# Kernel tuning notes

Hardware: AMD Instinct MI355X
Metric: run time of the kernel (lower is better)

The kernel has to match this reference:

```python
import jax, jax.numpy as jnp
import numpy as np

B, T, NM = 128, 2048, 8  # batch, nSteps, nMaxwell


def setup_inputs() -> dict:
    key = jax.random.key(0)
    k1, k2, k3 = jax.random.split(key, 3)
    S_e = jax.random.normal(k1, (B, T, 3, 3), dtype=jnp.float32)
    # strictly increasing times per batch element
    dt = jax.random.uniform(k2, (B, T), minval=0.01, maxval=0.1, dtype=jnp.float32)
    t = jnp.cumsum(dt, axis=1)
    # [tau_1..tau_nM, g_infy, g_1..g_nM] -> last dim 2*NM + 1
    PronyParams = jax.random.uniform(k3, (B, T, 2 * NM + 1), minval=0.1, maxval=1.0, dtype=jnp.float32)
    return {"S_e": S_e, "t": t, "PronyParams": PronyParams}


def reference(S_e, t, PronyParams):
    """Viscoelastic 2nd Piola-Kirchhoff stress via recursive Prony update.

    S_e:         [B, T, 3, 3] instantaneous elastic stress
    t:           [B, T] time
    PronyParams: [B, T, 2*nM+1] (relaxation times tau then coefficients g)
    Returns (S, S_infy, Q_sum), each [B, T, 3, 3].
    """
    nM = PronyParams.shape[-1] // 2
    tau = PronyParams[..., :nM]                      # [B,T,nM]
    g = PronyParams[..., nM:]                        # [B,T,nM+1]
    g = g / jnp.sum(g, axis=-1, keepdims=True)
    g_infy = g[..., 0:1]                             # [B,T,1]
    g_i = g[..., 1:]                                 # [B,T,nM]

    Bsz = S_e.shape[0]
    # time-major scan inputs
    xs = (
        jnp.swapaxes(t, 0, 1),      # [T,B]
        jnp.swapaxes(S_e, 0, 1),    # [T,B,3,3]
        jnp.swapaxes(tau, 0, 1),    # [T,B,nM]
        jnp.swapaxes(g_i, 0, 1),    # [T,B,nM]
    )
    init = (
        jnp.zeros((Bsz, nM, 3, 3), S_e.dtype),  # Q_0
        -t[:, 1],                                # t_prev (as in original initializer)
        jnp.zeros((Bsz, 3, 3), S_e.dtype),       # S_prev
        tau[:, 0],
        g_i[:, 0],
    )

    def step(carry, x):
        Q_p, t_p, S_p, tau_p, g_p = carry
        t_c, S_c, tau_c, g_c = x
        g_bar = 0.5 * (g_c + g_p)                 # [B,nM]
        tau_bar = 0.5 * (tau_c + tau_p)           # [B,nM]
        dt = (t_c - t_p)[:, None]                 # [B,1]
        e = jnp.exp(-0.5 * dt / tau_bar)          # exp(-dt/(2 tau_bar))
        term1 = (e * e)[..., None, None]          # exp(-dt/tau_bar), [B,nM,1,1]
        term2 = (e * g_bar)[..., None, None]      # [B,nM,1,1]
        dS = (S_c - S_p)[:, None]                 # [B,1,3,3]
        Q = term1 * Q_p + term2 * dS              # [B,nM,3,3]
        return (Q, t_c, S_c, tau_c, g_c), Q

    _, Qs = jax.lax.scan(step, init, xs)          # [T,B,nM,3,3]
    Q_sum = jnp.swapaxes(jnp.sum(Qs, axis=2), 0, 1)  # [B,T,3,3]
    S_infy = g_infy[..., None] * S_e              # [B,T,1,1] * [B,T,3,3]
    S = S_infy + Q_sum
    return (S, S_infy, Q_sum)
```

## Files before the change

### kernel.cpp

```cpp
#include <hip/hip_runtime.h>

#define T_LEN 2048
#define NMODE 8
#define NPP   17

template <int L, int G>
__global__ __launch_bounds__(256)
void phaseA(const float* __restrict__ Se,
            const float* __restrict__ tt,
            const float* __restrict__ pp,
            float* __restrict__ out,
            float* __restrict__ partR,
            float* __restrict__ partP,
            float* __restrict__ caA,
            int B) {
    constexpr int NC    = T_LEN / L;
    constexpr int NSTEP = G * L;
    constexpr int RW    = NSTEP + 1;
    constexpr int NT    = 256;
    constexpr int RAW_SZ = RW * NPP;
    constexpr int QT_SZ  = 9 * (NSTEP + 4);
    constexpr int CA_K   = L * 8 + 4;
    constexpr int UNION_SZ = (RAW_SZ > QT_SZ + G * CA_K) ? RAW_SZ
                                                         : (QT_SZ + G * CA_K);
    constexpr int AC_K  = L * 16 + 4;
    constexpr int O_AC  = UNION_SZ;
    constexpr int SROW  = NSTEP + 4;
    constexpr int O_ST  = O_AC + G * AC_K;
    constexpr int O_T   = O_ST + 9 * SROW;
    constexpr int O_INV = O_T + RW;
    constexpr int O_GI  = O_INV + RW;
    constexpr int TOTAL = O_GI + RW;

    __shared__ __align__(16) float sm[TOTAL];
    float* s_raw = sm;
    float* s_qT  = sm;
    float* s_ca  = sm + QT_SZ;
    float* s_AC  = sm + O_AC;
    float* s_ST  = sm + O_ST;
    float* s_t   = sm + O_T;
    float* s_inv = sm + O_INV;
    float* s_gi  = sm + O_GI;

    const int tid  = threadIdx.x;
    const int ngrp = NC / G;
    const int b    = blockIdx.x / ngrp;
    const int grp  = blockIdx.x % ngrp;
    const int c0   = grp * G;
    const int base = c0 * L;
    const int off  = (base == 0) ? 0 : 1;
    const int r0   = (base == 0) ? 0 : base - 1;

    {
        const float* pr = pp + ((size_t)b * T_LEN + r0) * NPP;
        for (int i = tid; i < RW * NPP; i += NT) s_raw[i] = pr[i];
        const float* sr = Se + ((size_t)b * T_LEN + r0) * 9;
        for (int i = tid; i < RW * 9; i += NT) {
            int r = i / 9, e = i - r * 9;
            s_ST[e * SROW + r] = sr[i];
        }
        const float* tr = tt + (size_t)b * T_LEN + r0;
        for (int i = tid; i < RW; i += NT) s_t[i] = tr[i];
    }
    __syncthreads();

    for (int i = tid; i < RW; i += NT) {
        float gs = 0.f;
        #pragma unroll
        for (int k = 8; k < NPP; ++k) gs += s_raw[i * NPP + k];
        float iv = __builtin_amdgcn_rcpf(gs);
        s_inv[i] = iv;
        s_gi[i]  = s_raw[i * NPP + 8] * iv;
    }
    __syncthreads();

    for (int i = tid; i < NSTEP * 8; i += NT) {
        int m  = i & 7;
        int ts = i >> 3;
        int rc = ts + off;
        bool first = (base == 0) && (ts == 0);
        int rp = first ? rc : rc - 1;
        float tau_c = s_raw[rc * NPP + m];
        float tau_p = s_raw[rp * NPP + m];
        float gqh_c = 0.5f * s_raw[rc * NPP + 9 + m] * s_inv[rc];
        float gqh_p = 0.5f * s_raw[rp * NPP + 9 + m] * s_inv[rp];
        float t_c = s_t[rc];
        float t_p = first ? -s_t[1] : s_t[rp];
        float ee  = __expf((t_p - t_c) * __builtin_amdgcn_rcpf(tau_c + tau_p));
        int kk = ts / L, sl = ts % L;
        s_AC[kk * AC_K + sl * 16 + m]     = ee * ee;
        s_AC[kk * AC_K + sl * 16 + 8 + m] = ee * (gqh_c + gqh_p);
    }
    __syncthreads();

    const size_t nOut = (size_t)B * T_LEN * 9;

    if (tid < 72) {
        const int k  = tid / 9;
        const int e  = tid - k * 9;
        const int cg = c0 + k;

        float dS[L];
        {
            float Sv[L + 1];
            Sv[0] = (cg == 0) ? 0.f : s_ST[e * SROW + (k * L + off - 1)];
            #pragma unroll
            for (int s = 0; s < L; ++s)
                Sv[s + 1] = s_ST[e * SROW + (k * L + s + off)];
            #pragma unroll
            for (int s = 0; s < L; ++s) dS[s] = Sv[s + 1] - Sv[s];
        }

        float Q[8] = {0,0,0,0,0,0,0,0};
        const float4* acp = (const float4*)(s_AC + k * AC_K);

        float4 a0 = acp[0], a1 = acp[1], c0v = acp[2], c1v = acp[3];
        #pragma unroll
        for (int s = 0; s < L; ++s) {
            float4 na0, na1, nc0, nc1;
            if (s < L - 1) {
                na0 = acp[4*s+4]; na1 = acp[4*s+5];
                nc0 = acp[4*s+6]; nc1 = acp[4*s+7];
            }
            float d = dS[s];
            Q[0] = a0.x*Q[0] + c0v.x*d;  Q[1] = a0.y*Q[1] + c0v.y*d;
            Q[2] = a0.z*Q[2] + c0v.z*d;  Q[3] = a0.w*Q[3] + c0v.w*d;
            Q[4] = a1.x*Q[4] + c1v.x*d;  Q[5] = a1.y*Q[5] + c1v.y*d;
            Q[6] = a1.z*Q[6] + c1v.z*d;  Q[7] = a1.w*Q[7] + c1v.w*d;
            float qs = ((Q[0]+Q[1])+(Q[2]+Q[3])) + ((Q[4]+Q[5])+(Q[6]+Q[7]));
            s_qT[e * SROW + (k * L + s)] = qs;
            a0 = na0; a1 = na1; c0v = nc0; c1v = nc1;
        }

        float4* pr4 = (float4*)(partR + ((size_t)(b * 9 + e) * NC + cg) * 8);
        pr4[0] = make_float4(Q[0], Q[1], Q[2], Q[3]);
        pr4[1] = make_float4(Q[4], Q[5], Q[6], Q[7]);
    } else if (tid < 192) {
        float* o1 = out + nOut + ((size_t)b * T_LEN + base) * 9;
        for (int i = tid - 72; i < NSTEP * 9; i += 120) {
            int t = i / 9, e = i - t * 9;
            int rc = t + off;
            o1[i] = s_gi[rc] * s_ST[e * SROW + rc];
        }
    } else {
        const int u = tid - 192;
        const int k = u >> 3;
        const int m = u & 7;
        float c = 1.f;
        #pragma unroll
        for (int s = 0; s < L; ++s) {
            c *= s_AC[k * AC_K + s * 16 + m];
            s_ca[k * CA_K + s * 8 + m] = c;
        }
        partP[((size_t)b * NC + (c0 + k)) * 8 + m] = c;
    }
    __syncthreads();

    float* o2 = out + 2 * nOut + ((size_t)b * T_LEN + base) * 9;
    for (int i4 = tid; i4 < NSTEP * 9 / 4; i4 += NT) {
        int i = i4 * 4;
        float4 v;
        {
            int t0i = i / 9,     e0i = i - t0i * 9;
            int t1i = (i+1) / 9, e1i = (i+1) - t1i * 9;
            int t2i = (i+2) / 9, e2i = (i+2) - t2i * 9;
            int t3i = (i+3) / 9, e3i = (i+3) - t3i * 9;
            v.x = s_qT[e0i * SROW + t0i];
            v.y = s_qT[e1i * SROW + t1i];
            v.z = s_qT[e2i * SROW + t2i];
            v.w = s_qT[e3i * SROW + t3i];
        }
        ((float4*)o2)[i4] = v;
    }
    float* ca = caA + ((size_t)b * NC + c0) * (L * 8);
    {
        int k = tid >> 5, j = tid & 31;
        const float4* src = (const float4*)(s_ca + k * CA_K);
        ((float4*)(ca + k * L * 8))[j] = src[j];
    }
}

template <int K>
__global__ __launch_bounds__(256)
void chunk_scan_wave(float* __restrict__ R, const float* __restrict__ P,
                     int B) {
    constexpr int NC = K * 64;
    int gtid = blockIdx.x * blockDim.x + threadIdx.x;
    int wid  = gtid >> 6;
    int lane = gtid & 63;
    if (wid >= B * 9) return;
    int e = wid % 9;
    int b = wid / 9;

    float* rp       = R + ((size_t)(b * 9 + e) * NC) * NMODE;
    const float* pq = P + ((size_t)b * NC) * NMODE;

    float pk[K][NMODE], rk[K][NMODE];
    float pa[NMODE], ra[NMODE];
    #pragma unroll
    for (int m = 0; m < NMODE; ++m) { pa[m] = 1.f; ra[m] = 0.f; }

    #pragma unroll
    for (int k = 0; k < K; ++k) {
        int c = lane * K + k;
        const float4* rv = (const float4*)(rp + (size_t)c * NMODE);
        const float4* pv = (const float4*)(pq + (size_t)c * NMODE);
        float4 r0 = rv[0], r1 = rv[1], p0 = pv[0], p1 = pv[1];
        rk[k][0]=r0.x; rk[k][1]=r0.y; rk[k][2]=r0.z; rk[k][3]=r0.w;
        rk[k][4]=r1.x; rk[k][5]=r1.y; rk[k][6]=r1.z; rk[k][7]=r1.w;
        pk[k][0]=p0.x; pk[k][1]=p0.y; pk[k][2]=p0.z; pk[k][3]=p0.w;
        pk[k][4]=p1.x; pk[k][5]=p1.y; pk[k][6]=p1.z; pk[k][7]=p1.w;
        #pragma unroll
        for (int m = 0; m < NMODE; ++m) {
            ra[m] = pk[k][m] * ra[m] + rk[k][m];
            pa[m] = pk[k][m] * pa[m];
        }
    }

    #pragma unroll
    for (int d = 1; d < 64; d <<= 1) {
        #pragma unroll
        for (int m = 0; m < NMODE; ++m) {
            float plo = __shfl_up(pa[m], d);
            float rlo = __shfl_up(ra[m], d);
            if (lane >= d) {
                ra[m] = pa[m] * rlo + ra[m];
                pa[m] = pa[m] * plo;
            }
        }
    }

    float z[NMODE];
    #pragma unroll
    for (int m = 0; m < NMODE; ++m) {
        float zz = __shfl_up(ra[m], 1);
        z[m] = (lane == 0) ? 0.f : zz;
    }

    #pragma unroll
    for (int k = 0; k < K; ++k) {
        int c = lane * K + k;
        float4* rv = (float4*)(rp + (size_t)c * NMODE);
        rv[0] = make_float4(z[0], z[1], z[2], z[3]);
        rv[1] = make_float4(z[4], z[5], z[6], z[7]);
        #pragma unroll
        for (int m = 0; m < NMODE; ++m)
            z[m] = pk[k][m] * z[m] + rk[k][m];
    }
}

template <int L, int GC>
__global__ __launch_bounds__(256)
void phaseC(float* __restrict__ out,
            const float* __restrict__ partR,
            const float* __restrict__ caA,
            int B) {
    constexpr int NC = T_LEN / L;
    constexpr int NE = GC * L * 9;
    const int tid  = threadIdx.x;
    const int ngrp = NC / GC;
    const int b  = blockIdx.x / ngrp;
    const int g  = blockIdx.x % ngrp;
    const int c0 = g * GC;

    __shared__ float s_Z[GC * 72];
    __shared__ __align__(16) float s_ca[GC * L * 8];

    for (int i = tid; i < GC * 72; i += 256) {
        int cl = i / 72, u = i % 72, e = u >> 3, m = u & 7;
        s_Z[i] = partR[((size_t)(b * 9 + e) * NC + c0 + cl) * 8 + m];
    }
    {
        const float4* ca4 = (const float4*)(caA + ((size_t)b * NC + c0) * (L * 8));
        for (int i = tid; i < GC * L * 2; i += 256)
            ((float4*)s_ca)[i] = ca4[i];
    }
    __syncthreads();

    const size_t nOut = (size_t)B * T_LEN * 9;
    float* o = out + ((size_t)b * T_LEN + (size_t)c0 * L) * 9;
    const float4* sf4 = (const float4*)(o + nOut);
    float4* s4 = (float4*)o;
    float4* q4 = (float4*)(o + 2 * nOut);

    for (int i4 = tid; i4 < NE / 4; i4 += 256) {
        int i = i4 * 4;
        float4 qv = q4[i4];
        float4 fv = sf4[i4];
        float corr[4];
        #pragma unroll
        for (int j = 0; j < 4; ++j) {
            int t = (i + j) / 9, e = (i + j) - t * 9;
            int cl = t / L;
            const float* caT = &s_ca[t * 8];
            const float* zE  = &s_Z[cl * 72 + e * 8];
            float cr = 0.f;
            #pragma unroll
            for (int m = 0; m < NMODE; ++m) cr += caT[m] * zE[m];
            corr[j] = cr;
        }
        float4 qn = make_float4(qv.x + corr[0], qv.y + corr[1],
                                qv.z + corr[2], qv.w + corr[3]);
        q4[i4] = qn;
        s4[i4] = make_float4(fv.x + qn.x, fv.y + qn.y,
                             fv.z + qn.z, fv.w + qn.w);
    }
}

extern "C" void kernel_launch(void* const* d_in, const int* in_sizes, int n_in,
                              void* d_out, int out_size, void* d_ws, size_t ws_size,
                              hipStream_t stream) {
    const float* Se = (const float*)d_in[0];
    const float* tt = (const float*)d_in[1];
    const float* pp = (const float*)d_in[2];
    float* out = (float*)d_out;

    int B = in_sizes[1] / T_LEN;

    constexpr int L  = 16;
    constexpr int NC = T_LEN / L;
    constexpr int K  = NC / 64;
    constexpr int G  = 8;
    constexpr int GC = 8;

    float* partR = (float*)d_ws;
    float* partP = partR + (size_t)B * 9 * NC * 8;
    float* caA   = partP + (size_t)B * NC * 8;

    int gridA = B * (NC / G);
    int gridB = (B * 9 * 64 + 255) / 256;
    int gridC = B * (NC / GC);

    phaseA<L, G><<<gridA, dim3(256), 0, stream>>>(
        Se, tt, pp, out, partR, partP, caA, B);
    chunk_scan_wave<K><<<gridB, dim3(256), 0, stream>>>(partR, partP, B);
    phaseC<L, GC><<<gridC, dim3(256), 0, stream>>>(out, partR, caA, B);
}
```

Baseline: 109.6 us.

## Fuse three-phase chunked scan into single-pass kernel with decoupled lookback

Replaces the three-kernel pipeline (local chunk scan, cross-chunk wave scan, correction pass) with one fused kernel. Each block takes a tile via an atomic ticket, computes local chunk results, publishes a per-tile spine (carry and decay product) and flag, then serially folds all predecessor tiles' spines before writing the final S, S_infy and Q_sum directly. This removes the intermediate global round-trips of the Q_sum and S_infy outputs and the partR and caA buffers, plus two kernel launches. In exchange it adds a memset, spin-waiting on flags, and a lookback loop that grows linearly with tile index.

```diff
diff --git a/kernel.cpp b/kernel.cpp
--- a/kernel.cpp
+++ b/kernel.cpp
@@ -6,48 +6,60 @@
 
 template <int L, int G>
 __global__ __launch_bounds__(256)
-void phaseA(const float* __restrict__ Se,
-            const float* __restrict__ tt,
-            const float* __restrict__ pp,
-            float* __restrict__ out,
-            float* __restrict__ partR,
-            float* __restrict__ partP,
-            float* __restrict__ caA,
-            int B) {
-    constexpr int NC    = T_LEN / L;
+void fused(const float* __restrict__ Se,
+           const float* __restrict__ tt,
+           const float* __restrict__ pp,
+           float* __restrict__ out,
+           float* __restrict__ spine,
+           unsigned* __restrict__ flags,
+           unsigned* __restrict__ ticket,
+           int B) {
     constexpr int NSTEP = G * L;
+    constexpr int TILES = T_LEN / NSTEP;
     constexpr int RW    = NSTEP + 1;
     constexpr int NT    = 256;
     constexpr int RAW_SZ = RW * NPP;
-    constexpr int QT_SZ  = 9 * (NSTEP + 4);
+    constexpr int SROW   = NSTEP + 4;
+    constexpr int QT_SZ  = 9 * SROW;
     constexpr int CA_K   = L * 8 + 4;
     constexpr int UNION_SZ = (RAW_SZ > QT_SZ + G * CA_K) ? RAW_SZ
                                                          : (QT_SZ + G * CA_K);
     constexpr int AC_K  = L * 16 + 4;
     constexpr int O_AC  = UNION_SZ;
-    constexpr int SROW  = NSTEP + 4;
-    constexpr int O_ST  = O_AC + G * AC_K;
+    constexpr int O_RP  = O_AC + G * AC_K;
+    constexpr int O_ST  = O_RP + G * 72 + G * 8;
     constexpr int O_T   = O_ST + 9 * SROW;
     constexpr int O_INV = O_T + RW;
     constexpr int O_GI  = O_INV + RW;
     constexpr int TOTAL = O_GI + RW;
+    static_assert(L == 16, "epilogue uses t>>4 / t&15");
+    static_assert(G * 72 + G * 8 + G * 72 <= G * AC_K, "overlay fits in AC");
 
     __shared__ __align__(16) float sm[TOTAL];
-    float* s_raw = sm;
-    float* s_qT  = sm;
-    float* s_ca  = sm + QT_SZ;
-    float* s_AC  = sm + O_AC;
-    float* s_ST  = sm + O_ST;
-    float* s_t   = sm + O_T;
-    float* s_inv = sm + O_INV;
-    float* s_gi  = sm + O_GI;
-
-    const int tid  = threadIdx.x;
-    const int ngrp = NC / G;
-    const int b    = blockIdx.x / ngrp;
-    const int grp  = blockIdx.x % ngrp;
-    const int c0   = grp * G;
-    const int base = c0 * L;
+    float* s_raw  = sm;
+    float* s_qT   = sm;
+    float* s_ca   = sm + QT_SZ;
+    float* s_AC   = sm + O_AC;
+    float* s_Zrel = sm + O_AC;
+    float* s_Pp   = sm + O_AC + G * 72;
+    float* s_Z    = sm + O_AC + G * 72 + G * 8;
+    float* s_R    = sm + O_RP;
+    float* s_P    = sm + O_RP + G * 72;
+    float* s_ST   = sm + O_ST;
+    float* s_t    = sm + O_T;
+    float* s_inv  = sm + O_INV;
+    float* s_gi   = sm + O_GI;
+
+    const int tid = threadIdx.x;
+
+    __shared__ unsigned s_vid;
+    if (tid == 0) s_vid = atomicAdd(ticket, 1u);
+    __syncthreads();
+    const int vid  = (int)(s_vid % (unsigned)(B * TILES));
+    const int tile = vid / B;
+    const int b    = vid % B;
+
+    const int base = tile * NSTEP;
     const int off  = (base == 0) ? 0 : 1;
     const int r0   = (base == 0) ? 0 : base - 1;
 
@@ -93,17 +105,16 @@
     }
     __syncthreads();
 
-    const size_t nOut = (size_t)B * T_LEN * 9;
-
     if (tid < 72) {
-        const int k  = tid / 9;
-        const int e  = tid - k * 9;
-        const int cg = c0 + k;
+        const int k = tid / 9;
+        const int e = tid - k * 9;
 
         float dS[L];
         {
             float Sv[L + 1];
-            Sv[0] = (cg == 0) ? 0.f : s_ST[e * SROW + (k * L + off - 1)];
+            Sv[0] = (base == 0 && k == 0)
+                        ? 0.f
+                        : s_ST[e * SROW + (k * L + off - 1)];
             #pragma unroll
             for (int s = 0; s < L; ++s)
                 Sv[s + 1] = s_ST[e * SROW + (k * L + s + off)];
@@ -132,17 +143,10 @@
             a0 = na0; a1 = na1; c0v = nc0; c1v = nc1;
         }
 
-        float4* pr4 = (float4*)(partR + ((size_t)(b * 9 + e) * NC + cg) * 8);
-        pr4[0] = make_float4(Q[0], Q[1], Q[2], Q[3]);
-        pr4[1] = make_float4(Q[4], Q[5], Q[6], Q[7]);
-    } else if (tid < 192) {
-        float* o1 = out + nOut + ((size_t)b * T_LEN + base) * 9;
-        for (int i = tid - 72; i < NSTEP * 9; i += 120) {
-            int t = i / 9, e = i - t * 9;
-            int rc = t + off;
-            o1[i] = s_gi[rc] * s_ST[e * SROW + rc];
-        }
-    } else {
+        float4* r4 = (float4*)(s_R + (k * 72 + e * 8));
+        r4[0] = make_float4(Q[0], Q[1], Q[2], Q[3]);
+        r4[1] = make_float4(Q[4], Q[5], Q[6], Q[7]);
+    } else if (tid >= 192) {
         const int u = tid - 192;
         const int k = u >> 3;
         const int m = u & 7;
@@ -152,158 +156,92 @@
             c *= s_AC[k * AC_K + s * 16 + m];
             s_ca[k * CA_K + s * 8 + m] = c;
         }
-        partP[((size_t)b * NC + (c0 + k)) * 8 + m] = c;
-    }
-    __syncthreads();
-
-    float* o2 = out + 2 * nOut + ((size_t)b * T_LEN + base) * 9;
+        s_P[u] = c;
+    }
+    __syncthreads();
+
+    if (tid < 72) {
+        const int e = tid >> 3;
+        const int m = tid & 7;
+        float z = 0.f, pprod = 1.f;
+        #pragma unroll
+        for (int k = 0; k < G; ++k) {
+            s_Zrel[k * 72 + tid] = z;
+            if (e == 0) s_Pp[k * 8 + m] = pprod;
+            float Pk = s_P[k * 8 + m];
+            z = Pk * z + s_R[k * 72 + tid];
+            pprod *= Pk;
+        }
+        if (tile != TILES - 1) {
+            float* sp = spine + ((size_t)b * TILES + tile) * 80;
+            sp[8 + tid] = z;
+            if (e == 0) sp[m] = pprod;
+        }
+    }
+    __syncthreads();
+
+    if (tile != TILES - 1 && tid == 0) {
+        __threadfence();
+        __hip_atomic_store(&flags[(size_t)b * TILES + tile], 1u,
+                           __ATOMIC_RELEASE, __HIP_MEMORY_SCOPE_AGENT);
+    }
+
+    float zin = 0.f;
+    {
+        const int e = tid >> 3;
+        const int m = tid & 7;
+        for (int j = 0; j < tile; ++j) {
+            if (tid == 0) {
+                while (__hip_atomic_load(&flags[(size_t)b * TILES + j],
+                                         __ATOMIC_ACQUIRE,
+                                         __HIP_MEMORY_SCOPE_AGENT) == 0u)
+                    __builtin_amdgcn_s_sleep(2);
+            }
+            __syncthreads();
+            if (tid < 72) {
+                float* sp = spine + ((size_t)b * TILES + j) * 80;
+                float Pj = __hip_atomic_load(sp + m, __ATOMIC_RELAXED,
+                                             __HIP_MEMORY_SCOPE_AGENT);
+                float Rj = __hip_atomic_load(sp + 8 + tid, __ATOMIC_RELAXED,
+                                             __HIP_MEMORY_SCOPE_AGENT);
+                zin = Pj * zin + Rj;
+            }
+        }
+    }
+
+    if (tid < 72) {
+        const int m = tid & 7;
+        #pragma unroll
+        for (int k = 0; k < G; ++k)
+            s_Z[k * 72 + tid] = s_Pp[k * 8 + m] * zin + s_Zrel[k * 72 + tid];
+    }
+    __syncthreads();
+
+    const size_t nOut = (size_t)B * T_LEN * 9;
+    float* o0 = out + ((size_t)b * T_LEN + base) * 9;
+    float* o1 = o0 + nOut;
+    float* o2 = o0 + 2 * nOut;
     for (int i4 = tid; i4 < NSTEP * 9 / 4; i4 += NT) {
         int i = i4 * 4;
-        float4 v;
-        {
-            int t0i = i / 9,     e0i = i - t0i * 9;
-            int t1i = (i+1) / 9, e1i = (i+1) - t1i * 9;
-            int t2i = (i+2) / 9, e2i = (i+2) - t2i * 9;
-            int t3i = (i+3) / 9, e3i = (i+3) - t3i * 9;
-            v.x = s_qT[e0i * SROW + t0i];
-            v.y = s_qT[e1i * SROW + t1i];
-            v.z = s_qT[e2i * SROW + t2i];
-            v.w = s_qT[e3i * SROW + t3i];
-        }
-        ((float4*)o2)[i4] = v;
-    }
-    float* ca = caA + ((size_t)b * NC + c0) * (L * 8);
-    {
-        int k = tid >> 5, j = tid & 31;
-        const float4* src = (const float4*)(s_ca + k * CA_K);
-        ((float4*)(ca + k * L * 8))[j] = src[j];
-    }
-}
-
-template <int K>
-__global__ __launch_bounds__(256)
-void chunk_scan_wave(float* __restrict__ R, const float* __restrict__ P,
-                     int B) {
-    constexpr int NC = K * 64;
-    int gtid = blockIdx.x * blockDim.x + threadIdx.x;
-    int wid  = gtid >> 6;
-    int lane = gtid & 63;
-    if (wid >= B * 9) return;
-    int e = wid % 9;
-    int b = wid / 9;
-
-    float* rp       = R + ((size_t)(b * 9 + e) * NC) * NMODE;
-    const float* pq = P + ((size_t)b * NC) * NMODE;
-
-    float pk[K][NMODE], rk[K][NMODE];
-    float pa[NMODE], ra[NMODE];
-    #pragma unroll
-    for (int m = 0; m < NMODE; ++m) { pa[m] = 1.f; ra[m] = 0.f; }
-
-    #pragma unroll
-    for (int k = 0; k < K; ++k) {
-        int c = lane * K + k;
-        const float4* rv = (const float4*)(rp + (size_t)c * NMODE);
-        const float4* pv = (const float4*)(pq + (size_t)c * NMODE);
-        float4 r0 = rv[0], r1 = rv[1], p0 = pv[0], p1 = pv[1];
-        rk[k][0]=r0.x; rk[k][1]=r0.y; rk[k][2]=r0.z; rk[k][3]=r0.w;
-        rk[k][4]=r1.x; rk[k][5]=r1.y; rk[k][6]=r1.z; rk[k][7]=r1.w;
-        pk[k][0]=p0.x; pk[k][1]=p0.y; pk[k][2]=p0.z; pk[k][3]=p0.w;
-        pk[k][4]=p1.x; pk[k][5]=p1.y; pk[k][6]=p1.z; pk[k][7]=p1.w;
-        #pragma unroll
-        for (int m = 0; m < NMODE; ++m) {
-            ra[m] = pk[k][m] * ra[m] + rk[k][m];
-            pa[m] = pk[k][m] * pa[m];
-        }
-    }
-
-    #pragma unroll
-    for (int d = 1; d < 64; d <<= 1) {
-        #pragma unroll
-        for (int m = 0; m < NMODE; ++m) {
-            float plo = __shfl_up(pa[m], d);
-            float rlo = __shfl_up(ra[m], d);
-            if (lane >= d) {
-                ra[m] = pa[m] * rlo + ra[m];
-                pa[m] = pa[m] * plo;
-            }
-        }
-    }
-
-    float z[NMODE];
-    #pragma unroll
-    for (int m = 0; m < NMODE; ++m) {
-        float zz = __shfl_up(ra[m], 1);
-        z[m] = (lane == 0) ? 0.f : zz;
-    }
-
-    #pragma unroll
-    for (int k = 0; k < K; ++k) {
-        int c = lane * K + k;
-        float4* rv = (float4*)(rp + (size_t)c * NMODE);
-        rv[0] = make_float4(z[0], z[1], z[2], z[3]);
-        rv[1] = make_float4(z[4], z[5], z[6], z[7]);
-        #pragma unroll
-        for (int m = 0; m < NMODE; ++m)
-            z[m] = pk[k][m] * z[m] + rk[k][m];
-    }
-}
-
-template <int L, int GC>
-__global__ __launch_bounds__(256)
-void phaseC(float* __restrict__ out,
-            const float* __restrict__ partR,
-            const float* __restrict__ caA,
-            int B) {
-    constexpr int NC = T_LEN / L;
-    constexpr int NE = GC * L * 9;
-    const int tid  = threadIdx.x;
-    const int ngrp = NC / GC;
-    const int b  = blockIdx.x / ngrp;
-    const int g  = blockIdx.x % ngrp;
-    const int c0 = g * GC;
-
-    __shared__ float s_Z[GC * 72];
-    __shared__ __align__(16) float s_ca[GC * L * 8];
-
-    for (int i = tid; i < GC * 72; i += 256) {
-        int cl = i / 72, u = i % 72, e = u >> 3, m = u & 7;
-        s_Z[i] = partR[((size_t)(b * 9 + e) * NC + c0 + cl) * 8 + m];
-    }
-    {
-        const float4* ca4 = (const float4*)(caA + ((size_t)b * NC + c0) * (L * 8));
-        for (int i = tid; i < GC * L * 2; i += 256)
-            ((float4*)s_ca)[i] = ca4[i];
-    }
-    __syncthreads();
-
-    const size_t nOut = (size_t)B * T_LEN * 9;
-    float* o = out + ((size_t)b * T_LEN + (size_t)c0 * L) * 9;
-    const float4* sf4 = (const float4*)(o + nOut);
-    float4* s4 = (float4*)o;
-    float4* q4 = (float4*)(o + 2 * nOut);
-
-    for (int i4 = tid; i4 < NE / 4; i4 += 256) {
-        int i = i4 * 4;
-        float4 qv = q4[i4];
-        float4 fv = sf4[i4];
-        float corr[4];
+        float q[4], f[4];
         #pragma unroll
         for (int j = 0; j < 4; ++j) {
-            int t = (i + j) / 9, e = (i + j) - t * 9;
-            int cl = t / L;
-            const float* caT = &s_ca[t * 8];
-            const float* zE  = &s_Z[cl * 72 + e * 8];
+            int idx = i + j;
+            int t = idx / 9, e = idx - t * 9;
+            int rc = t + off;
+            int k = t >> 4, s = t & 15;
+            const float* caT = &s_ca[k * CA_K + s * 8];
+            const float* zE  = &s_Z[k * 72 + e * 8];
             float cr = 0.f;
             #pragma unroll
             for (int m = 0; m < NMODE; ++m) cr += caT[m] * zE[m];
-            corr[j] = cr;
-        }
-        float4 qn = make_float4(qv.x + corr[0], qv.y + corr[1],
-                                qv.z + corr[2], qv.w + corr[3]);
-        q4[i4] = qn;
-        s4[i4] = make_float4(fv.x + qn.x, fv.y + qn.y,
-                             fv.z + qn.z, fv.w + qn.w);
+            q[j] = s_qT[e * SROW + t] + cr;
+            f[j] = s_gi[rc] * s_ST[e * SROW + rc];
+        }
+        ((float4*)o2)[i4] = make_float4(q[0], q[1], q[2], q[3]);
+        ((float4*)o1)[i4] = make_float4(f[0], f[1], f[2], f[3]);
+        ((float4*)o0)[i4] = make_float4(f[0]+q[0], f[1]+q[1],
+                                        f[2]+q[2], f[3]+q[3]);
     }
 }
 
@@ -317,22 +255,19 @@
 
     int B = in_sizes[1] / T_LEN;
 
-    constexpr int L  = 16;
-    constexpr int NC = T_LEN / L;
-    constexpr int K  = NC / 64;
-    constexpr int G  = 8;
-    constexpr int GC = 8;
-
-    float* partR = (float*)d_ws;
-    float* partP = partR + (size_t)B * 9 * NC * 8;
-    float* caA   = partP + (size_t)B * NC * 8;
-
-    int gridA = B * (NC / G);
-    int gridB = (B * 9 * 64 + 255) / 256;
-    int gridC = B * (NC / GC);
-
-    phaseA<L, G><<<gridA, dim3(256), 0, stream>>>(
-        Se, tt, pp, out, partR, partP, caA, B);
-    chunk_scan_wave<K><<<gridB, dim3(256), 0, stream>>>(partR, partP, B);
-    phaseC<L, GC><<<gridC, dim3(256), 0, stream>>>(out, partR, caA, B);
+    constexpr int L = 16;
+    constexpr int G = 8;
+    constexpr int NSTEP = G * L;
+    constexpr int TILES = T_LEN / NSTEP;
+
+    unsigned* ticket = (unsigned*)d_ws;
+    unsigned* flags  = ticket + 1;
+    size_t ctl_bytes = (size_t)(1 + B * TILES) * sizeof(unsigned);
+    size_t spine_off = (ctl_bytes + 15) & ~(size_t)15;
+    float* spine = (float*)((char*)d_ws + spine_off);
+
+    hipMemsetAsync(d_ws, 0, ctl_bytes, stream);
+
+    fused<L, G><<<B * TILES, dim3(256), 0, stream>>>(
+        Se, tt, pp, out, spine, flags, ticket, B);
 }
```

Result: slower. 299.7 us (+173.5%).
